# Performance work log

Hardware: AMD Instinct MI355X
Metric: run time of the kernel (lower is better)

## Reference

```python
import jax, jax.numpy as jnp
import numpy as np

LEVELS = 16
FEATURES = 2
HASHMAP_SIZE = 524288
BASE_RES = 16
PER_LEVEL_SCALE = 1.5
HIDDEN = 64
N_POINTS = 2097152
IN_DIM = LEVELS * FEATURES + 3  # 35

# per-level integer resolutions, computed exactly like int(base_res * scale**l)
RES = jnp.asarray([int(BASE_RES * PER_LEVEL_SCALE ** l) for l in range(LEVELS)], dtype=jnp.float32)

P1, P2, P3 = np.int32(73856093), np.int32(19349663), np.int32(83492791)


def hash_coords(coords):
    # coords: [..., 3] int32. int32 multiply wraps, matching torch .int() semantics.
    h = (coords[..., 0] * P1) ^ (coords[..., 1] * P2) ^ (coords[..., 2] * P3)
    return jnp.mod(h, HASHMAP_SIZE)  # Python-style mod -> non-negative


def setup_inputs() -> dict:
    key = jax.random.key(0)
    ks = jax.random.split(key, 8)
    x = jax.random.uniform(ks[0], (N_POINTS, 3), dtype=jnp.float32)
    view_dir = jax.random.normal(ks[1], (N_POINTS, 3), dtype=jnp.float32)
    tables = jax.random.normal(ks[2], (LEVELS, HASHMAP_SIZE, FEATURES), dtype=jnp.float32) * 0.01
    W0 = jax.random.normal(ks[3], (IN_DIM, HIDDEN), dtype=jnp.float32) * (1.0 / np.sqrt(IN_DIM))
    b0 = jnp.zeros((HIDDEN,), jnp.float32)
    W1 = jax.random.normal(ks[4], (HIDDEN, HIDDEN), dtype=jnp.float32) * (1.0 / np.sqrt(HIDDEN))
    b1 = jnp.zeros((HIDDEN,), jnp.float32)
    W2 = jax.random.normal(ks[5], (HIDDEN, 4), dtype=jnp.float32) * (1.0 / np.sqrt(HIDDEN))
    b2 = jnp.zeros((4,), jnp.float32)
    return {"x": x, "view_dir": view_dir, "tables": tables,
            "W0": W0, "b0": b0, "W1": W1, "b1": b1, "W2": W2, "b2": b2}


def reference(x, view_dir, tables, W0, b0, W1, b1, W2, b2):
    # Hash-grid encoding, vectorized over levels: pos [L, N, 3]
    pos = x[None, :, :] * RES[:, None, None]
    pos_floor = jnp.floor(pos).astype(jnp.int32)
    idx = hash_coords(pos_floor)                      # [L, N]
    emb = jax.vmap(lambda t, i: t[i])(tables, idx)    # [L, N, F]
    h = jnp.transpose(emb, (1, 0, 2)).reshape(x.shape[0], LEVELS * FEATURES)
    h = jnp.concatenate([h, view_dir], axis=-1)       # [N, 35]
    h = jax.nn.relu(h @ W0 + b0)
    h = jax.nn.relu(h @ W1 + b1)
    out = h @ W2 + b2                                  # [N, 4]
    rgb = jax.nn.sigmoid(out[..., :3])
    sigma = jax.nn.relu(out[..., 3:4])
    return rgb, sigma
```

## Files before the change

kernel.cpp:

```cpp
#include <hip/hip_runtime.h>
#include <math.h>

#define LEVELS 16
#define HASHMAP_SIZE (1 << 19)
#define N_POINTS 2097152

typedef __attribute__((ext_vector_type(8))) short bf16x8;
typedef __attribute__((ext_vector_type(4))) float f32x4;

__device__ __constant__ float c_res[LEVELS] = {
    16.f, 24.f, 36.f, 54.f, 81.f, 121.f, 182.f, 273.f,
    410.f, 615.f, 922.f, 1383.f, 2075.f, 3113.f, 4670.f, 7006.f};

__device__ __forceinline__ unsigned short f2bf(float f) {
    unsigned u = __builtin_bit_cast(unsigned, f);
    u += 0x7FFFu + ((u >> 16) & 1u);
    return (unsigned short)(u >> 16);
}
__device__ __forceinline__ float bf2f(unsigned short s) {
    unsigned u = ((unsigned)s) << 16;
    return __builtin_bit_cast(float, u);
}

__device__ __forceinline__ unsigned swz(unsigned row, unsigned colbyte) {
    return row * 128u + (colbyte ^ ((row & 7u) << 4));
}

__device__ __forceinline__ unsigned hash3(float px, float py, float pz, float r) {
    const int ix = (int)floorf(px * r);
    const int iy = (int)floorf(py * r);
    const int iz = (int)floorf(pz * r);
    const unsigned h = (unsigned)ix * 73856093u
                     ^ (unsigned)iy * 19349663u
                     ^ (unsigned)iz * 83492791u;
    return h & (unsigned)(HASHMAP_SIZE - 1);
}

__device__ __forceinline__ bf16x8 load_wfrag(const float* __restrict__ W, int ncols,
                                             int n, int k0, int kmax) {
    bf16x8 r;
    #pragma unroll
    for (int j = 0; j < 8; ++j) {
        const int k = k0 + j;
        const float v = (k < kmax) ? W[k * ncols + n] : 0.f;
        r[j] = (short)f2bf(v);
    }
    return r;
}

__global__ __launch_bounds__(256) void conv_tables(const float* __restrict__ tables,
                                                   unsigned* __restrict__ tabp) {
    const int t = blockIdx.x * 256 + threadIdx.x;
    const float4 a = *reinterpret_cast<const float4*>(tables + (size_t)t * 8);
    const float4 b = *reinterpret_cast<const float4*>(tables + (size_t)t * 8 + 4);
    uint4 o;
    o.x = (unsigned)f2bf(a.x) | ((unsigned)f2bf(a.y) << 16);
    o.y = (unsigned)f2bf(a.z) | ((unsigned)f2bf(a.w) << 16);
    o.z = (unsigned)f2bf(b.x) | ((unsigned)f2bf(b.y) << 16);
    o.w = (unsigned)f2bf(b.z) | ((unsigned)f2bf(b.w) << 16);
    *reinterpret_cast<uint4*>(tabp + (size_t)t * 4) = o;
}

__global__ __launch_bounds__(256) void conv_weights(const float* __restrict__ W0,
                                                    const float* __restrict__ W1,
                                                    unsigned short* __restrict__ w0p,
                                                    unsigned short* __restrict__ w1p) {
    for (int i = threadIdx.x; i < 4096; i += 256) {
        const int n = i >> 6, k = i & 63;
        w0p[n * 64 + k] = f2bf((k < 35) ? W0[k * 64 + n] : 0.f);
        w1p[n * 64 + k] = f2bf(W1[k * 64 + n]);
    }
}

__global__ __launch_bounds__(256, 8) void nerf_gather(
    const float* __restrict__ x,
    const unsigned* __restrict__ tabp,
    unsigned* __restrict__ feat,
    int chunkbase, int chunkpts)
{
    const int b = blockIdx.x;
    const int pair = b & 7;
    const int chunkblk = b >> 3;
    const int l0 = pair, l1 = pair + 8;
    const float r0 = c_res[l0], r1 = c_res[l1];
    const int tid = threadIdx.x;
    const int pbase = chunkblk * 2048;

    unsigned idxA[8], idxB[8];
    #pragma unroll
    for (int i = 0; i < 8; ++i) {
        const int pl = pbase + i * 256 + tid;
        const size_t pg = (size_t)chunkbase + pl;
        const float px = x[pg * 3 + 0];
        const float py = x[pg * 3 + 1];
        const float pz = x[pg * 3 + 2];
        idxA[i] = hash3(px, py, pz, r0);
        idxB[i] = hash3(px, py, pz, r1);
    }
    unsigned gA[8], gB[8];
    #pragma unroll
    for (int i = 0; i < 8; ++i) {
        gA[i] = tabp[(size_t)l0 * HASHMAP_SIZE + idxA[i]];
        gB[i] = tabp[(size_t)l1 * HASHMAP_SIZE + idxB[i]];
    }
    #pragma unroll
    for (int i = 0; i < 8; ++i) {
        const int pl = pbase + i * 256 + tid;
        feat[(size_t)l0 * chunkpts + pl] = gA[i];
        feat[(size_t)l1 * chunkpts + pl] = gB[i];
    }
}

__global__ __launch_bounds__(256, 4) void nerf_mlp(
    const unsigned* __restrict__ feat,
    const float* __restrict__ view_dir,
    const unsigned short* __restrict__ w0p,
    const unsigned short* __restrict__ w1p,
    const float* __restrict__ b0, const float* __restrict__ b1,
    const float* __restrict__ W2, const float* __restrict__ b2,
    float* __restrict__ out,
    int chunkbase, int chunkpts)
{
    __shared__ __align__(16) unsigned short acts[256 * 64];
    char* const actsb = (char*)acts;

    const int tid = threadIdx.x;
    const int gl = blockIdx.x * 256 + tid;
    const size_t gid = (size_t)chunkbase + gl;

    unsigned fw[18];
    #pragma unroll
    for (int l = 0; l < LEVELS; ++l)
        fw[l] = feat[(size_t)l * chunkpts + gl];
    fw[16] = (unsigned)f2bf(view_dir[gid * 3 + 0])
           | ((unsigned)f2bf(view_dir[gid * 3 + 1]) << 16);
    fw[17] = (unsigned)f2bf(view_dir[gid * 3 + 2]);

    {
        const unsigned row = (unsigned)tid;
        #pragma unroll
        for (int c = 0; c < 8; ++c) {
            int4 v;
            if (c < 4)       v = make_int4((int)fw[4*c], (int)fw[4*c+1], (int)fw[4*c+2], (int)fw[4*c+3]);
            else if (c == 4) v = make_int4((int)fw[16], (int)fw[17], 0, 0);
            else             v = make_int4(0, 0, 0, 0);
            *(int4*)(actsb + swz(row, (unsigned)(c * 16))) = v;
        }
    }

    const int lane = tid & 63;
    const int lr = lane & 15;
    const int lg = lane >> 4;
    const unsigned Rbase = (unsigned)(tid & ~63);

    #pragma unroll
    for (int layer = 0; layer < 2; ++layer) {
        const unsigned short* const Wp = layer ? w1p : w0p;
        const float* const bg = layer ? b1 : b0;

        bf16x8 bw[8];
        #pragma unroll
        for (int nt = 0; nt < 4; ++nt)
            #pragma unroll
            for (int ks = 0; ks < 2; ++ks)
                bw[nt * 2 + ks] = *(const bf16x8*)(Wp + (nt * 16 + lr) * 64 + (ks * 32 + lg * 8));

        #pragma unroll
        for (int rt = 0; rt < 4; ++rt) {
            bf16x8 aa[2];
            #pragma unroll
            for (int ks = 0; ks < 2; ++ks) {
                const unsigned row = Rbase + (unsigned)(rt * 16 + lr);
                aa[ks] = *(const bf16x8*)(actsb + swz(row, (unsigned)((ks * 4 + lg) * 16)));
            }
            #pragma unroll
            for (int nt = 0; nt < 4; ++nt) {
                const float bv = bg[nt * 16 + lr];
                f32x4 c = {bv, bv, bv, bv};
                c = __builtin_amdgcn_mfma_f32_16x16x32_bf16(aa[0], bw[nt * 2 + 0], c, 0, 0, 0);
                c = __builtin_amdgcn_mfma_f32_16x16x32_bf16(aa[1], bw[nt * 2 + 1], c, 0, 0, 0);
                #pragma unroll
                for (int r = 0; r < 4; ++r) {
                    const float v = fmaxf(c[r], 0.f);
                    const unsigned row = Rbase + (unsigned)(rt * 16 + lg * 4 + r);
                    const unsigned col = (unsigned)(nt * 16 + lr);
                    *(unsigned short*)(actsb + swz(row, col * 2)) = f2bf(v);
                }
            }
        }
    }

    {
        float o0 = b2[0], o1 = b2[1], o2 = b2[2], o3 = b2[3];
        const unsigned row = (unsigned)tid;
        #pragma unroll
        for (int c = 0; c < 8; ++c) {
            const bf16x8 v = *(const bf16x8*)(actsb + swz(row, (unsigned)(c * 16)));
            #pragma unroll
            for (int j = 0; j < 8; ++j) {
                const float s = bf2f((unsigned short)v[j]);
                const int k = c * 8 + j;
                o0 += s * W2[k * 4 + 0];
                o1 += s * W2[k * 4 + 1];
                o2 += s * W2[k * 4 + 2];
                o3 += s * W2[k * 4 + 3];
            }
        }
        out[gid * 3 + 0] = 1.f / (1.f + __expf(-o0));
        out[gid * 3 + 1] = 1.f / (1.f + __expf(-o1));
        out[gid * 3 + 2] = 1.f / (1.f + __expf(-o2));
        out[(size_t)N_POINTS * 3 + gid] = fmaxf(o3, 0.f);
    }
}

__global__ __launch_bounds__(256, 4) void nerf_fused(
    const float* __restrict__ x,
    const float* __restrict__ view_dir,
    const float* __restrict__ tables,
    const float* __restrict__ W0, const float* __restrict__ b0,
    const float* __restrict__ W1, const float* __restrict__ b1,
    const float* __restrict__ W2, const float* __restrict__ b2,
    float* __restrict__ out)
{
    __shared__ __align__(16) unsigned short acts[256 * 64];
    char* const actsb = (char*)acts;
    const int tid = threadIdx.x;
    const int gid = blockIdx.x * 256 + tid;
    const float px = x[gid * 3 + 0], py = x[gid * 3 + 1], pz = x[gid * 3 + 2];

    unsigned idx[LEVELS];
    #pragma unroll
    for (int l = 0; l < LEVELS; ++l) idx[l] = hash3(px, py, pz, c_res[l]);
    float2 f[LEVELS];
    #pragma unroll
    for (int l = 0; l < LEVELS; ++l)
        f[l] = *reinterpret_cast<const float2*>(tables + ((size_t)l * HASHMAP_SIZE + idx[l]) * 2);

    unsigned fw[18];
    #pragma unroll
    for (int l = 0; l < LEVELS; ++l)
        fw[l] = (unsigned)f2bf(f[l].x) | ((unsigned)f2bf(f[l].y) << 16);
    fw[16] = (unsigned)f2bf(view_dir[gid * 3 + 0])
           | ((unsigned)f2bf(view_dir[gid * 3 + 1]) << 16);
    fw[17] = (unsigned)f2bf(view_dir[gid * 3 + 2]);
    {
        const unsigned row = (unsigned)tid;
        #pragma unroll
        for (int c = 0; c < 8; ++c) {
            int4 v;
            if (c < 4)       v = make_int4((int)fw[4*c], (int)fw[4*c+1], (int)fw[4*c+2], (int)fw[4*c+3]);
            else if (c == 4) v = make_int4((int)fw[16], (int)fw[17], 0, 0);
            else             v = make_int4(0, 0, 0, 0);
            *(int4*)(actsb + swz(row, (unsigned)(c * 16))) = v;
        }
    }
    const int lane = tid & 63;
    const int lr = lane & 15;
    const int lg = lane >> 4;
    const unsigned Rbase = (unsigned)(tid & ~63);
    #pragma unroll
    for (int layer = 0; layer < 2; ++layer) {
        const float* const Wg = layer ? W1 : W0;
        const float* const bg = layer ? b1 : b0;
        const int kmax = layer ? 64 : 35;
        bf16x8 bw[8];
        #pragma unroll
        for (int nt = 0; nt < 4; ++nt)
            #pragma unroll
            for (int ks = 0; ks < 2; ++ks)
                bw[nt * 2 + ks] = load_wfrag(Wg, 64, nt * 16 + lr, ks * 32 + lg * 8, kmax);
        #pragma unroll
        for (int rt = 0; rt < 4; ++rt) {
            bf16x8 aa[2];
            #pragma unroll
            for (int ks = 0; ks < 2; ++ks) {
                const unsigned row = Rbase + (unsigned)(rt * 16 + lr);
                aa[ks] = *(const bf16x8*)(actsb + swz(row, (unsigned)((ks * 4 + lg) * 16)));
            }
            #pragma unroll
            for (int nt = 0; nt < 4; ++nt) {
                const float bv = bg[nt * 16 + lr];
                f32x4 c = {bv, bv, bv, bv};
                c = __builtin_amdgcn_mfma_f32_16x16x32_bf16(aa[0], bw[nt * 2 + 0], c, 0, 0, 0);
                c = __builtin_amdgcn_mfma_f32_16x16x32_bf16(aa[1], bw[nt * 2 + 1], c, 0, 0, 0);
                #pragma unroll
                for (int r = 0; r < 4; ++r) {
                    const float v = fmaxf(c[r], 0.f);
                    const unsigned row = Rbase + (unsigned)(rt * 16 + lg * 4 + r);
                    const unsigned col = (unsigned)(nt * 16 + lr);
                    *(unsigned short*)(actsb + swz(row, col * 2)) = f2bf(v);
                }
            }
        }
    }
    {
        float o0 = b2[0], o1 = b2[1], o2 = b2[2], o3 = b2[3];
        const unsigned row = (unsigned)tid;
        #pragma unroll
        for (int c = 0; c < 8; ++c) {
            const bf16x8 v = *(const bf16x8*)(actsb + swz(row, (unsigned)(c * 16)));
            #pragma unroll
            for (int j = 0; j < 8; ++j) {
                const float s = bf2f((unsigned short)v[j]);
                const int k = c * 8 + j;
                o0 += s * W2[k * 4 + 0];
                o1 += s * W2[k * 4 + 1];
                o2 += s * W2[k * 4 + 2];
                o3 += s * W2[k * 4 + 3];
            }
        }
        out[(size_t)gid * 3 + 0] = 1.f / (1.f + __expf(-o0));
        out[(size_t)gid * 3 + 1] = 1.f / (1.f + __expf(-o1));
        out[(size_t)gid * 3 + 2] = 1.f / (1.f + __expf(-o2));
        out[(size_t)N_POINTS * 3 + gid] = fmaxf(o3, 0.f);
    }
}

extern "C" void kernel_launch(void* const* d_in, const int* in_sizes, int n_in,
                              void* d_out, int out_size, void* d_ws, size_t ws_size,
                              hipStream_t stream) {
    (void)in_sizes; (void)n_in; (void)out_size;
    const float* x        = (const float*)d_in[0];
    const float* view_dir = (const float*)d_in[1];
    const float* tables   = (const float*)d_in[2];
    const float* W0       = (const float*)d_in[3];
    const float* b0       = (const float*)d_in[4];
    const float* W1       = (const float*)d_in[5];
    const float* b1       = (const float*)d_in[6];
    const float* W2       = (const float*)d_in[7];
    const float* b2       = (const float*)d_in[8];
    float* out = (float*)d_out;

    const size_t TAB_BYTES = (size_t)LEVELS * HASHMAP_SIZE * 4;
    const size_t WP_BYTES  = 16384;

    int nchunks = 0;
    if      (ws_size >= TAB_BYTES + WP_BYTES + (size_t)N_POINTS * 64) nchunks = 1;
    else if (ws_size >= TAB_BYTES + WP_BYTES + (size_t)N_POINTS * 32) nchunks = 2;
    else if (ws_size >= TAB_BYTES + WP_BYTES + (size_t)N_POINTS * 16) nchunks = 4;

    if (nchunks == 0) {
        nerf_fused<<<N_POINTS / 256, 256, 0, stream>>>(x, view_dir, tables,
                                                       W0, b0, W1, b1, W2, b2, out);
        return;
    }

    unsigned* tabp        = (unsigned*)d_ws;
    unsigned short* w0p   = (unsigned short*)((char*)d_ws + TAB_BYTES);
    unsigned short* w1p   = w0p + 4096;
    unsigned* feat        = (unsigned*)((char*)d_ws + TAB_BYTES + WP_BYTES);
    const int chunkpts = N_POINTS / nchunks;

    conv_tables<<<(LEVELS * HASHMAP_SIZE / 4) / 256, 256, 0, stream>>>(tables, tabp);
    conv_weights<<<1, 256, 0, stream>>>(W0, W1, w0p, w1p);

    for (int c = 0; c < nchunks; ++c) {
        const int base = c * chunkpts;
        nerf_gather<<<8 * (chunkpts / 2048), 256, 0, stream>>>(x, tabp, feat, base, chunkpts);
        nerf_mlp<<<chunkpts / 256, 256, 0, stream>>>(feat, view_dir, w0p, w1p,
                                                     b0, b1, W2, b2, out,
                                                     base, chunkpts);
    }
}
```

Baseline: 341.8 us.

## Move final MLP layer onto MFMA, pack bf16 conversion, fold weight conversion kernel

The last 64->4 layer now runs on MFMA instructions with zero-padded weight fragments instead of a per-thread scalar FMA loop over 64 inputs. Results are staged through shared memory as floats so each thread reads back its own row. The hidden-layer stores use a hardware packed bf16 convert instead of manual rounding. The separate one-block weight-conversion kernel is merged into the table-conversion kernel to save a launch. The MFMA path wastes 12 of 16 output columns and adds extra LDS traffic and a possible cross-wave ordering hazard on the shared buffer.

```diff
diff --git a/kernel.cpp b/kernel.cpp
--- a/kernel.cpp
+++ b/kernel.cpp
@@ -20,6 +20,11 @@
 __device__ __forceinline__ float bf2f(unsigned short s) {
     unsigned u = ((unsigned)s) << 16;
     return __builtin_bit_cast(float, u);
+}
+__device__ __forceinline__ unsigned cvt_pk_bf16(float a, float b) {
+    unsigned r;
+    asm("v_cvt_pk_bf16_f32 %0, %1, %2" : "=v"(r) : "v"(a), "v"(b));
+    return r;
 }
 
 __device__ __forceinline__ unsigned swz(unsigned row, unsigned colbyte) {
@@ -49,8 +54,18 @@
 }
 
 __global__ __launch_bounds__(256) void conv_tables(const float* __restrict__ tables,
-                                                   unsigned* __restrict__ tabp) {
+                                                   unsigned* __restrict__ tabp,
+                                                   const float* __restrict__ W0,
+                                                   const float* __restrict__ W1,
+                                                   unsigned short* __restrict__ w0p,
+                                                   unsigned short* __restrict__ w1p) {
     const int t = blockIdx.x * 256 + threadIdx.x;
+    if (blockIdx.x < 16) {
+        const int i = t;
+        const int n = i >> 6, k = i & 63;
+        w0p[n * 64 + k] = f2bf((k < 35) ? W0[k * 64 + n] : 0.f);
+        w1p[n * 64 + k] = f2bf(W1[k * 64 + n]);
+    }
     const float4 a = *reinterpret_cast<const float4*>(tables + (size_t)t * 8);
     const float4 b = *reinterpret_cast<const float4*>(tables + (size_t)t * 8 + 4);
     uint4 o;
@@ -59,17 +74,6 @@
     o.z = (unsigned)f2bf(b.x) | ((unsigned)f2bf(b.y) << 16);
     o.w = (unsigned)f2bf(b.z) | ((unsigned)f2bf(b.w) << 16);
     *reinterpret_cast<uint4*>(tabp + (size_t)t * 4) = o;
-}
-
-__global__ __launch_bounds__(256) void conv_weights(const float* __restrict__ W0,
-                                                    const float* __restrict__ W1,
-                                                    unsigned short* __restrict__ w0p,
-                                                    unsigned short* __restrict__ w1p) {
-    for (int i = threadIdx.x; i < 4096; i += 256) {
-        const int n = i >> 6, k = i & 63;
-        w0p[n * 64 + k] = f2bf((k < 35) ? W0[k * 64 + n] : 0.f);
-        w1p[n * 64 + k] = f2bf(W1[k * 64 + n]);
-    }
 }
 
 __global__ __launch_bounds__(256, 8) void nerf_gather(
@@ -179,37 +183,53 @@
                 f32x4 c = {bv, bv, bv, bv};
                 c = __builtin_amdgcn_mfma_f32_16x16x32_bf16(aa[0], bw[nt * 2 + 0], c, 0, 0, 0);
                 c = __builtin_amdgcn_mfma_f32_16x16x32_bf16(aa[1], bw[nt * 2 + 1], c, 0, 0, 0);
+                const unsigned u01 = cvt_pk_bf16(fmaxf(c[0], 0.f), fmaxf(c[1], 0.f));
+                const unsigned u23 = cvt_pk_bf16(fmaxf(c[2], 0.f), fmaxf(c[3], 0.f));
+                const unsigned col = (unsigned)(nt * 16 + lr);
+                const unsigned rbase = Rbase + (unsigned)(rt * 16 + lg * 4);
+                *(unsigned short*)(actsb + swz(rbase + 0, col * 2)) = (unsigned short)u01;
+                *(unsigned short*)(actsb + swz(rbase + 1, col * 2)) = (unsigned short)(u01 >> 16);
+                *(unsigned short*)(actsb + swz(rbase + 2, col * 2)) = (unsigned short)u23;
+                *(unsigned short*)(actsb + swz(rbase + 3, col * 2)) = (unsigned short)(u23 >> 16);
+            }
+        }
+    }
+
+    {
+        const bool valid = (lr < 4);
+        bf16x8 bw2[2];
+        #pragma unroll
+        for (int ks = 0; ks < 2; ++ks) {
+            if (valid) bw2[ks] = load_wfrag(W2, 4, lr, ks * 32 + lg * 8, 64);
+            else       bw2[ks] = bf16x8{0,0,0,0,0,0,0,0};
+        }
+        const float bc = valid ? b2[lr] : 0.f;
+
+        #pragma unroll
+        for (int rt = 0; rt < 4; ++rt) {
+            bf16x8 aa[2];
+            #pragma unroll
+            for (int ks = 0; ks < 2; ++ks) {
+                const unsigned row = Rbase + (unsigned)(rt * 16 + lr);
+                aa[ks] = *(const bf16x8*)(actsb + swz(row, (unsigned)((ks * 4 + lg) * 16)));
+            }
+            f32x4 c = {bc, bc, bc, bc};
+            c = __builtin_amdgcn_mfma_f32_16x16x32_bf16(aa[0], bw2[0], c, 0, 0, 0);
+            c = __builtin_amdgcn_mfma_f32_16x16x32_bf16(aa[1], bw2[1], c, 0, 0, 0);
+            if (valid) {
                 #pragma unroll
                 for (int r = 0; r < 4; ++r) {
-                    const float v = fmaxf(c[r], 0.f);
                     const unsigned row = Rbase + (unsigned)(rt * 16 + lg * 4 + r);
-                    const unsigned col = (unsigned)(nt * 16 + lr);
-                    *(unsigned short*)(actsb + swz(row, col * 2)) = f2bf(v);
+                    *(float*)(actsb + row * 128u + ((row & 7u) << 4) + (unsigned)lr * 4u) = c[r];
                 }
             }
         }
-    }
-
-    {
-        float o0 = b2[0], o1 = b2[1], o2 = b2[2], o3 = b2[3];
         const unsigned row = (unsigned)tid;
-        #pragma unroll
-        for (int c = 0; c < 8; ++c) {
-            const bf16x8 v = *(const bf16x8*)(actsb + swz(row, (unsigned)(c * 16)));
-            #pragma unroll
-            for (int j = 0; j < 8; ++j) {
-                const float s = bf2f((unsigned short)v[j]);
-                const int k = c * 8 + j;
-                o0 += s * W2[k * 4 + 0];
-                o1 += s * W2[k * 4 + 1];
-                o2 += s * W2[k * 4 + 2];
-                o3 += s * W2[k * 4 + 3];
-            }
-        }
-        out[gid * 3 + 0] = 1.f / (1.f + __expf(-o0));
-        out[gid * 3 + 1] = 1.f / (1.f + __expf(-o1));
-        out[gid * 3 + 2] = 1.f / (1.f + __expf(-o2));
-        out[(size_t)N_POINTS * 3 + gid] = fmaxf(o3, 0.f);
+        const f32x4 o = *(const f32x4*)(actsb + row * 128u + ((row & 7u) << 4));
+        out[gid * 3 + 0] = 1.f / (1.f + __expf(-o[0]));
+        out[gid * 3 + 1] = 1.f / (1.f + __expf(-o[1]));
+        out[gid * 3 + 2] = 1.f / (1.f + __expf(-o[2]));
+        out[(size_t)N_POINTS * 3 + gid] = fmaxf(o[3], 0.f);
     }
 }
 
@@ -351,8 +371,8 @@
     unsigned* feat        = (unsigned*)((char*)d_ws + TAB_BYTES + WP_BYTES);
     const int chunkpts = N_POINTS / nchunks;
 
-    conv_tables<<<(LEVELS * HASHMAP_SIZE / 4) / 256, 256, 0, stream>>>(tables, tabp);
-    conv_weights<<<1, 256, 0, stream>>>(W0, W1, w0p, w1p);
+    conv_tables<<<(LEVELS * HASHMAP_SIZE / 4) / 256, 256, 0, stream>>>(tables, tabp,
+                                                                      W0, W1, w0p, w1p);
 
     for (int c = 0; c < nchunks; ++c) {
         const int base = c * chunkpts;
```

Result: faster. 326.1 us (-4.6%).
